# Kernel optimization log

Measured on AMD Instinct MI355X. Metric: run time of the kernel, lower is better.

The kernel has to match this reference:

```python
import jax, jax.numpy as jnp
import numpy as np

B, S, D, DA, H = 4, 2048, 1024, 1024, 16
DH = DA // H  # 64, per-head dim (tensor_split on last dim == contiguous head chunks)


def setup_inputs() -> dict:
    key = jax.random.key(0)
    ks = jax.random.split(key, 8)
    init = 0.02
    return {
        "q": jax.random.normal(ks[0], (B, S, D), jnp.float32),
        "k": jax.random.normal(ks[1], (B, S, D), jnp.float32),
        "v": jax.random.normal(ks[2], (B, S, D), jnp.float32),
        "mask": jnp.ones((B, 1, S), jnp.int32),
        "w_q": jax.random.normal(ks[3], (DA, D), jnp.float32) * init,
        "b_q": jnp.zeros((DA,), jnp.float32),
        "w_k": jax.random.normal(ks[4], (DA, D), jnp.float32) * init,
        "b_k": jnp.zeros((DA,), jnp.float32),
        "w_v": jax.random.normal(ks[5], (DA, D), jnp.float32) * init,
        "b_v": jnp.zeros((DA,), jnp.float32),
        "w_o": jax.random.normal(ks[6], (D, DA), jnp.float32) * init,
        "b_o": jnp.zeros((D,), jnp.float32),
    }


def reference(q, k, v, mask, w_q, b_q, w_k, b_k, w_v, b_v, w_o, b_o):
    # projections (nn.Linear: x @ W.T + b)
    xq = q @ w_q.T + b_q            # [B,S,DA]
    xk = k @ w_k.T + b_k
    xv = v @ w_v.T + b_v
    # tensor_split into h contiguous chunks == reshape to [B,S,H,DH]
    xq = xq.reshape(B, S, H, DH)
    xk = xk.reshape(B, S, H, DH)
    xv = xv.reshape(B, S, H, DH)
    scores = jnp.einsum('bqhd,bkhd->bhqk', xq, xk) / jnp.sqrt(jnp.asarray(DH, xq.dtype))
    # mask [B,1,S] broadcasts over heads and query rows -> [B,1,1,S]
    scores = jnp.where(mask[:, None] == 0, -jnp.inf, scores)
    probs = jax.nn.softmax(scores, axis=-1)  # dropout p=0.0 -> identity
    out = jnp.einsum('bhqk,bkhd->bqhd', probs, xv).reshape(B, S, DA)
    return out @ w_o.T + b_o        # [B,S,D]
```

## Files before the change

### kernel.cpp

```cpp
#include <hip/hip_runtime.h>
#include <hip/hip_bf16.h>
#include <cstdint>
#include <cstddef>

typedef __bf16 bf16;
typedef __attribute__((ext_vector_type(8))) __bf16 bf16x8;
typedef __attribute__((ext_vector_type(4))) __bf16 bf16x4;
typedef __attribute__((ext_vector_type(4))) float f32x4;
typedef __attribute__((ext_vector_type(4))) int i32x4;

#define MFMA_BF16(a, b, c) __builtin_amdgcn_mfma_f32_16x16x32_bf16((a), (b), (c), 0, 0, 0)

constexpr int CB = 4;
constexpr int CS = 2048;
constexpr int CD = 1024;
constexpr int CDA = 1024;
constexpr int CH = 16;
constexpr int CM = CB * CS;
constexpr int NT = CS / 64;

__global__ __launch_bounds__(256) void cvt_w4(
    const float* __restrict__ s0, const float* __restrict__ s1,
    const float* __restrict__ s2, const float* __restrict__ s3,
    bf16* __restrict__ dst)
{
    int bid = blockIdx.x;
    int m = bid >> 9;
    size_t li = ((size_t)(bid & 511) * 256 + threadIdx.x) * 8;
    const float* s = (m == 0) ? s0 : (m == 1) ? s1 : (m == 2) ? s2 : s3;
    f32x4 a = *(const f32x4*)(s + li);
    f32x4 c = *(const f32x4*)(s + li + 4);
    bf16x8 o;
#pragma unroll
    for (int j = 0; j < 4; ++j) { o[j] = (bf16)a[j]; o[4 + j] = (bf16)c[j]; }
    *(bf16x8*)(dst + (size_t)m * (CD * CDA) + li) = o;
}

struct P3 {
    const float *A0, *A1, *A2;
    const float *b0, *b1, *b2;
    bf16 *C0, *C1, *C2;
};

__global__ __launch_bounds__(512, 4) void gemm_proj(P3 p, const bf16* __restrict__ Wb)
{
    __shared__ __align__(16) char smem[49152];

    const int t = threadIdx.x;
    const int lane = t & 63;
    const int wid = t >> 6;
    const int wr = wid >> 2, wc = wid & 3;
    const int l15 = lane & 15, lg = lane >> 4;
    const int m0 = blockIdx.x * 128;
    const int n0 = blockIdx.y * 256;
    const int z = blockIdx.z;

    const float* A    = (z == 0) ? p.A0 : (z == 1) ? p.A1 : p.A2;
    const float* bias = (z == 0) ? p.b0 : (z == 1) ? p.b1 : p.b2;
    const bf16*  W    = Wb + (size_t)z * (CD * CDA);

    const int arow = t >> 2, aq = t & 3;
    const float* asrc = A + (size_t)(m0 + arow) * CD + aq * 16;
    const int aoff0 = arow * 128 + (((2 * aq) ^ (arow & 7)) << 4);
    const int aoff1 = arow * 128 + (((2 * aq + 1) ^ (arow & 7)) << 4);
    const int brow_ = wid * 8 + (lane >> 3);
    const int bcol = ((lane & 7) ^ ((lane >> 3) & 7)) << 3;

    char* Ab = smem;
    char* Bb = smem + 16384;

    f32x4 acc[4][4] = {};

    for (int ks = 0; ks < CD / 64; ++ks) {
        const int k0 = ks * 64;
        {
            f32x4 v0 = *(const f32x4*)(asrc + k0);
            f32x4 v1 = *(const f32x4*)(asrc + k0 + 4);
            bf16x8 o0;
#pragma unroll
            for (int jj = 0; jj < 4; ++jj) { o0[jj] = (bf16)v0[jj]; o0[4 + jj] = (bf16)v1[jj]; }
            *(bf16x8*)(Ab + aoff0) = o0;
        }
        {
            f32x4 v2 = *(const f32x4*)(asrc + k0 + 8);
            f32x4 v3 = *(const f32x4*)(asrc + k0 + 12);
            bf16x8 o1;
#pragma unroll
            for (int jj = 0; jj < 4; ++jj) { o1[jj] = (bf16)v2[jj]; o1[4 + jj] = (bf16)v3[jj]; }
            *(bf16x8*)(Ab + aoff1) = o1;
        }
#pragma unroll
        for (int i = 0; i < 4; ++i) {
            const bf16* src = W + (size_t)(n0 + i * 64 + brow_) * CD + k0 + bcol;
            __builtin_amdgcn_global_load_lds(
                (const __attribute__((address_space(1))) void*)src,
                (__attribute__((address_space(3))) void*)(Bb + i * 8192 + wid * 1024),
                16, 0, 0);
        }
        __syncthreads();

#pragma unroll
        for (int kk = 0; kk < 64; kk += 32) {
            bf16x8 af[4], bfv[4];
#pragma unroll
            for (int mi = 0; mi < 4; ++mi) {
                int row = wr * 64 + mi * 16 + l15;
                af[mi] = *(const bf16x8*)(Ab + row * 128 +
                                          ((((kk >> 3) + lg) ^ (row & 7)) << 4));
            }
#pragma unroll
            for (int ni = 0; ni < 4; ++ni) {
                int row = wc * 64 + ni * 16 + l15;
                bfv[ni] = *(const bf16x8*)(Bb + 128 * row +
                                           ((((kk >> 3) + lg) ^ (row & 7)) << 4));
            }
            __builtin_amdgcn_s_setprio(1);
#pragma unroll
            for (int mi = 0; mi < 4; ++mi)
#pragma unroll
                for (int ni = 0; ni < 4; ++ni)
                    acc[mi][ni] = MFMA_BF16(af[mi], bfv[ni], acc[mi][ni]);
            __builtin_amdgcn_s_setprio(0);
        }
        __syncthreads();
    }

    if (z == 2) {
        bf16* C = p.C2;
        const int mblock = m0 + wr * 64;
#pragma unroll
        for (int ni = 0; ni < 4; ++ni) {
            int n = n0 + wc * 64 + ni * 16 + l15;
            float bv = bias[n];
#pragma unroll
            for (int mi = 0; mi < 4; ++mi) {
                int s = mi * 16 + lg * 4;
                int cps = (s & 32) | ((s & 12) << 1) | ((s & 16) >> 2);
                bf16x4 o;
#pragma unroll
                for (int r = 0; r < 4; ++r) o[r] = (bf16)(acc[mi][ni][r] + bv);
                *(bf16x4*)(C + (size_t)n * CM + mblock + cps) = o;
            }
        }
    } else {
        bf16* C = (z == 0) ? p.C0 : p.C1;
#pragma unroll
        for (int ni = 0; ni < 4; ++ni) {
            int col = n0 + wc * 64 + ni * 16 + l15;
            float bv = bias[col];
#pragma unroll
            for (int mi = 0; mi < 4; ++mi)
#pragma unroll
                for (int r = 0; r < 4; ++r) {
                    int row = m0 + wr * 64 + mi * 16 + lg * 4 + r;
                    C[(size_t)row * CDA + col] = (bf16)(acc[mi][ni][r] + bv);
                }
        }
    }
}

__global__ __launch_bounds__(512, 4) void gemm_out(
    const bf16* __restrict__ A, const bf16* __restrict__ W,
    const float* __restrict__ bias, float* __restrict__ C)
{
    __shared__ __align__(16) char smem[49152];

    const int t = threadIdx.x;
    const int lane = t & 63;
    const int wid = t >> 6;
    const int wr = wid >> 2, wc = wid & 3;
    const int l15 = lane & 15, lg = lane >> 4;
    const int m0 = blockIdx.x * 128;
    const int n0 = blockIdx.y * 256;

    const int grow_ = wid * 8 + (lane >> 3);
    const int gcol = ((lane & 7) ^ ((lane >> 3) & 7)) << 3;

    char* Ab = smem;
    char* Bb = smem + 16384;

    f32x4 acc[4][4] = {};

    for (int ks = 0; ks < CDA / 64; ++ks) {
        const int k0 = ks * 64;
#pragma unroll
        for (int i = 0; i < 2; ++i) {
            const bf16* src = A + (size_t)(m0 + i * 64 + grow_) * CDA + k0 + gcol;
            __builtin_amdgcn_global_load_lds(
                (const __attribute__((address_space(1))) void*)src,
                (__attribute__((address_space(3))) void*)(Ab + i * 8192 + wid * 1024),
                16, 0, 0);
        }
#pragma unroll
        for (int i = 0; i < 4; ++i) {
            const bf16* src = W + (size_t)(n0 + i * 64 + grow_) * CDA + k0 + gcol;
            __builtin_amdgcn_global_load_lds(
                (const __attribute__((address_space(1))) void*)src,
                (__attribute__((address_space(3))) void*)(Bb + i * 8192 + wid * 1024),
                16, 0, 0);
        }
        __syncthreads();

#pragma unroll
        for (int kk = 0; kk < 64; kk += 32) {
            bf16x8 af[4], bfv[4];
#pragma unroll
            for (int mi = 0; mi < 4; ++mi) {
                int row = wr * 64 + mi * 16 + l15;
                af[mi] = *(const bf16x8*)(Ab + row * 128 +
                                          ((((kk >> 3) + lg) ^ (row & 7)) << 4));
            }
#pragma unroll
            for (int ni = 0; ni < 4; ++ni) {
                int row = wc * 64 + ni * 16 + l15;
                bfv[ni] = *(const bf16x8*)(Bb + 128 * row +
                                           ((((kk >> 3) + lg) ^ (row & 7)) << 4));
            }
            __builtin_amdgcn_s_setprio(1);
#pragma unroll
            for (int mi = 0; mi < 4; ++mi)
#pragma unroll
                for (int ni = 0; ni < 4; ++ni)
                    acc[mi][ni] = MFMA_BF16(af[mi], bfv[ni], acc[mi][ni]);
            __builtin_amdgcn_s_setprio(0);
        }
        __syncthreads();
    }

#pragma unroll
    for (int ni = 0; ni < 4; ++ni) {
        int col = n0 + wc * 64 + ni * 16 + l15;
        float bv = bias[col];
#pragma unroll
        for (int mi = 0; mi < 4; ++mi)
#pragma unroll
            for (int r = 0; r < 4; ++r) {
                int row = m0 + wr * 64 + mi * 16 + lg * 4 + r;
                C[(size_t)row * CD + col] = acc[mi][ni][r] + bv;
            }
    }
}

__global__ __launch_bounds__(512, 4) void attn_kernel(
    const bf16* __restrict__ xq, const bf16* __restrict__ xk,
    const bf16* __restrict__ xvT, const int* __restrict__ mask,
    bf16* __restrict__ out)
{
    __shared__ __align__(16) char smem[40960];
    float* Mb = (float*)(smem + 32768);

    const int t = threadIdx.x;
    const int lane = t & 63;
    const int wid = t >> 6;
    const int l15 = lane & 15, lg = lane >> 4;
    const int g = blockIdx.x;
    const int j = g >> 3;
    const int bh = (g & 7) * 8 + (j & 7);
    const int qt = j >> 3;
    const int b = bh >> 4, h = bh & 15;
    const int q0 = qt * 256;
    constexpr float SCL = 0.125f * 1.44269504088896340736f;
    constexpr float M2 = 12.0f * SCL;

    const int sub = lane >> 3;
    const int sb  = (lane & 7) ^ sub;
    const bf16* kbase = xk + (size_t)(b * CS + wid * 8 + sub) * CDA + h * 64 + sb * 8;
    const bf16* vbase = xvT + (size_t)(h * 64 + wid * 8 + sub) * CM + b * CS + sb * 8;

#define STAGE(bufi, ktt)                                                           \
    {                                                                              \
        char* Kd = smem + (bufi) * 16384 + wid * 1024;                             \
        char* Vd = smem + (bufi) * 16384 + 8192 + wid * 1024;                      \
        __builtin_amdgcn_global_load_lds(                                          \
            (const __attribute__((address_space(1))) void*)(kbase + (size_t)(ktt) * 64 * CDA), \
            (__attribute__((address_space(3))) void*)Kd, 16, 0, 0);                \
        __builtin_amdgcn_global_load_lds(                                          \
            (const __attribute__((address_space(1))) void*)(vbase + (ktt) * 64),   \
            (__attribute__((address_space(3))) void*)Vd, 16, 0, 0);                \
    }

    {
        i32x4 mk = *(const i32x4*)(mask + b * CS + t * 4);
        f32x4 o;
#pragma unroll
        for (int r = 0; r < 4; ++r) o[r] = (mk[r] == 0) ? -1.0e30f : -M2;
        *(f32x4*)(Mb + t * 4) = o;
    }

    bf16x8 aq[2][2];
#pragma unroll
    for (int mi = 0; mi < 2; ++mi)
#pragma unroll
        for (int kh = 0; kh < 2; ++kh) {
            bf16x8 v = *(const bf16x8*)(xq +
                (size_t)(b * CS + q0 + wid * 32 + mi * 16 + l15) * CDA + h * 64 + kh * 32 + lg * 8);
#pragma unroll
            for (int jj = 0; jj < 8; ++jj) v[jj] = (bf16)((float)v[jj] * SCL);
            aq[mi][kh] = v;
        }

    bf16x8 onescol;
    {
        bf16 fv = (l15 == 0) ? (bf16)1.0f : (bf16)0.0f;
#pragma unroll
        for (int jj = 0; jj < 8; ++jj) onescol[jj] = fv;
    }

    int koff[2][4], voff[2][4];
#pragma unroll
    for (int kh = 0; kh < 2; ++kh)
#pragma unroll
        for (int ni = 0; ni < 4; ++ni) {
            int key = ni * 16 + l15;
            koff[kh][ni] = key * 128 + ((kh * 64 + lg * 16) ^ ((key & 7) << 4));
        }
#pragma unroll
    for (int kks = 0; kks < 2; ++kks)
#pragma unroll
        for (int di = 0; di < 4; ++di) {
            int d = di * 16 + l15;
            voff[kks][di] = 8192 + d * 128 + ((kks * 64 + lg * 16) ^ ((d & 7) << 4));
        }

    f32x4 accO[2][5] = {};

    STAGE(0, 0);
    __syncthreads();

    for (int kt = 0; kt < NT; ++kt) {
        const int cur = kt & 1;
        char* buf = smem + cur * 16384;

        if (kt + 1 < NT) STAGE(cur ^ 1, kt + 1);

        f32x4 mb[4];
#pragma unroll
        for (int ni = 0; ni < 4; ++ni)
            mb[ni] = *(const f32x4*)(Mb + kt * 64 + ni * 16 + lg * 4);

        f32x4 sT[4][2];
#pragma unroll
        for (int ni = 0; ni < 4; ++ni) { sT[ni][0] = mb[ni]; sT[ni][1] = mb[ni]; }
#pragma unroll
        for (int kh = 0; kh < 2; ++kh) {
            bf16x8 bk[4];
#pragma unroll
            for (int ni = 0; ni < 4; ++ni)
                bk[ni] = *(const bf16x8*)(buf + koff[kh][ni]);
            __builtin_amdgcn_s_setprio(1);
#pragma unroll
            for (int ni = 0; ni < 4; ++ni)
#pragma unroll
                for (int mi = 0; mi < 2; ++mi)
                    sT[ni][mi] = MFMA_BF16(bk[ni], aq[mi][kh], sT[ni][mi]);
            __builtin_amdgcn_s_setprio(0);
        }

#pragma unroll
        for (int ni = 0; ni < 4; ++ni)
#pragma unroll
            for (int mi = 0; mi < 2; ++mi)
#pragma unroll
                for (int r = 0; r < 4; ++r)
                    sT[ni][mi][r] = exp2f(sT[ni][mi][r]);

        bf16x8 ap[2][2];
#pragma unroll
        for (int kks = 0; kks < 2; ++kks)
#pragma unroll
            for (int mi = 0; mi < 2; ++mi)
#pragma unroll
                for (int r = 0; r < 4; ++r) {
                    ap[kks][mi][r]     = (bf16)sT[2 * kks][mi][r];
                    ap[kks][mi][4 + r] = (bf16)sT[2 * kks + 1][mi][r];
                }

#pragma unroll
        for (int kks = 0; kks < 2; ++kks) {
            bf16x8 bv[4];
#pragma unroll
            for (int di = 0; di < 4; ++di)
                bv[di] = *(const bf16x8*)(buf + voff[kks][di]);
            __builtin_amdgcn_s_setprio(1);
#pragma unroll
            for (int mi = 0; mi < 2; ++mi) {
#pragma unroll
                for (int di = 0; di < 4; ++di)
                    accO[mi][di] = MFMA_BF16(ap[kks][mi], bv[di], accO[mi][di]);
                accO[mi][4] = MFMA_BF16(ap[kks][mi], onescol, accO[mi][4]);
            }
            __builtin_amdgcn_s_setprio(0);
        }

        __syncthreads();
    }
#undef STAGE

    char* Ob = smem + wid * 2048;
#pragma unroll
    for (int mi = 0; mi < 2; ++mi) {
#pragma unroll
        for (int r = 0; r < 4; ++r) {
            float lsum = __shfl(accO[mi][4][r], lane & 48);
            float inv = 1.0f / lsum;
            int qr = lg * 4 + r;
#pragma unroll
            for (int di = 0; di < 4; ++di)
                *(bf16*)(Ob + qr * 128 + (((di * 16 + l15) * 2) ^ ((qr & 7) << 4))) =
                    (bf16)(accO[mi][di][r] * inv);
        }
        __builtin_amdgcn_sched_barrier(0);
#pragma unroll
        for (int i = 0; i < 2; ++i) {
            int rr = i * 8 + (lane >> 3);
            int ch = lane & 7;
            bf16x8 o = *(const bf16x8*)(Ob + rr * 128 + ((ch * 16) ^ ((rr & 7) << 4)));
            *(bf16x8*)(out + (size_t)(b * CS + q0 + wid * 32 + mi * 16 + rr) * CDA +
                       h * 64 + ch * 8) = o;
        }
        __builtin_amdgcn_sched_barrier(0);
    }
}

extern "C" void kernel_launch(void* const* d_in, const int* in_sizes, int n_in,
                              void* d_out, int out_size, void* d_ws, size_t ws_size,
                              hipStream_t stream)
{
    const float* q   = (const float*)d_in[0];
    const float* k   = (const float*)d_in[1];
    const float* v   = (const float*)d_in[2];
    const int*   msk = (const int*)d_in[3];
    const float* w_q = (const float*)d_in[4];
    const float* b_q = (const float*)d_in[5];
    const float* w_k = (const float*)d_in[6];
    const float* b_k = (const float*)d_in[7];
    const float* w_v = (const float*)d_in[8];
    const float* b_v = (const float*)d_in[9];
    const float* w_o = (const float*)d_in[10];
    const float* b_o = (const float*)d_in[11];

    bf16* xq  = (bf16*)d_ws;
    bf16* xk  = xq + (size_t)CM * CDA;
    bf16* xvT = xk + (size_t)CM * CDA;
    bf16* at  = xvT + (size_t)CM * CDA;
    bf16* wb  = at + (size_t)CM * CDA;

    cvt_w4<<<dim3(2048), 256, 0, stream>>>(w_q, w_k, w_v, w_o, wb);

    P3 p{q, k, v, b_q, b_k, b_v, xq, xk, xvT};
    gemm_proj<<<dim3(CM / 128, CDA / 256, 3), 512, 0, stream>>>(p, wb);

    attn_kernel<<<dim3(512), 512, 0, stream>>>(xq, xk, xvT, msk, at);

    gemm_out<<<dim3(CM / 128, CD / 256), 512, 0, stream>>>(
        at, wb + 3 * (size_t)(CD * CDA), b_o, (float*)d_out);
}
```

Measured before the change: 197.4 us.

## Retile projection GEMM to 64x512 and double-buffer output GEMM LDS

The projection GEMM moves from 128x256 tiles to 64x512 tiles, with each of the 8 waves owning a 64-column strip. Each fp32 activation row is then read and converted once per 512 output columns rather than once per 256, which halves repeated A traffic and conversion work. The output GEMM gains a two-stage LDS ping-pong so the next k-slice loads while the current one is computed. The cost is larger shared memory use (72KB and 96KB) and fewer resident blocks per CU. The visible part of the output-GEMM loop does not show where the end-of-iteration synchronization sits.

```diff
diff --git a/kernel.cpp b/kernel.cpp
--- a/kernel.cpp
+++ b/kernel.cpp
@@ -44,7 +44,115 @@
 
 __global__ __launch_bounds__(512, 4) void gemm_proj(P3 p, const bf16* __restrict__ Wb)
 {
-    __shared__ __align__(16) char smem[49152];
+    __shared__ __align__(16) char smem[73728];
+
+    const int t = threadIdx.x;
+    const int lane = t & 63;
+    const int wid = t >> 6;
+    const int l15 = lane & 15, lg = lane >> 4;
+    const int m0 = blockIdx.x * 64;
+    const int n0 = blockIdx.y * 512;
+    const int z = blockIdx.z;
+
+    const float* A    = (z == 0) ? p.A0 : (z == 1) ? p.A1 : p.A2;
+    const float* bias = (z == 0) ? p.b0 : (z == 1) ? p.b1 : p.b2;
+    const bf16*  W    = Wb + (size_t)z * (CD * CDA);
+
+    const int arow = t >> 3, ac = t & 7;
+    const float* asrc = A + (size_t)(m0 + arow) * CD + ac * 8;
+    const int aoff = arow * 128 + ((ac ^ (arow & 7)) << 4);
+    const int brow_ = wid * 8 + (lane >> 3);
+    const int bcol = ((lane & 7) ^ ((lane >> 3) & 7)) << 3;
+
+    char* Ab = smem;
+    char* Bb = smem + 8192;
+
+    f32x4 acc[4][4] = {};
+
+    for (int ks = 0; ks < CD / 64; ++ks) {
+        const int k0 = ks * 64;
+        {
+            f32x4 v0 = *(const f32x4*)(asrc + k0);
+            f32x4 v1 = *(const f32x4*)(asrc + k0 + 4);
+            bf16x8 o;
+#pragma unroll
+            for (int jj = 0; jj < 4; ++jj) { o[jj] = (bf16)v0[jj]; o[4 + jj] = (bf16)v1[jj]; }
+            *(bf16x8*)(Ab + aoff) = o;
+        }
+#pragma unroll
+        for (int i = 0; i < 8; ++i) {
+            const bf16* src = W + (size_t)(n0 + i * 64 + brow_) * CD + k0 + bcol;
+            __builtin_amdgcn_global_load_lds(
+                (const __attribute__((address_space(1))) void*)src,
+                (__attribute__((address_space(3))) void*)(Bb + i * 8192 + wid * 1024),
+                16, 0, 0);
+        }
+        __syncthreads();
+
+#pragma unroll
+        for (int kk = 0; kk < 64; kk += 32) {
+            bf16x8 af[4], bfv[4];
+#pragma unroll
+            for (int mi = 0; mi < 4; ++mi) {
+                int row = mi * 16 + l15;
+                af[mi] = *(const bf16x8*)(Ab + row * 128 +
+                                          ((((kk >> 3) + lg) ^ (row & 7)) << 4));
+            }
+#pragma unroll
+            for (int ni = 0; ni < 4; ++ni) {
+                int row = wid * 64 + ni * 16 + l15;
+                bfv[ni] = *(const bf16x8*)(Bb + 128 * row +
+                                           ((((kk >> 3) + lg) ^ (row & 7)) << 4));
+            }
+            __builtin_amdgcn_s_setprio(1);
+#pragma unroll
+            for (int mi = 0; mi < 4; ++mi)
+#pragma unroll
+                for (int ni = 0; ni < 4; ++ni)
+                    acc[mi][ni] = MFMA_BF16(af[mi], bfv[ni], acc[mi][ni]);
+            __builtin_amdgcn_s_setprio(0);
+        }
+        __syncthreads();
+    }
+
+    if (z == 2) {
+        bf16* C = p.C2;
+#pragma unroll
+        for (int ni = 0; ni < 4; ++ni) {
+            int n = n0 + wid * 64 + ni * 16 + l15;
+            float bv = bias[n];
+#pragma unroll
+            for (int mi = 0; mi < 4; ++mi) {
+                int s = mi * 16 + lg * 4;
+                int cps = (s & 32) | ((s & 12) << 1) | ((s & 16) >> 2);
+                bf16x4 o;
+#pragma unroll
+                for (int r = 0; r < 4; ++r) o[r] = (bf16)(acc[mi][ni][r] + bv);
+                *(bf16x4*)(C + (size_t)n * CM + m0 + cps) = o;
+            }
+        }
+    } else {
+        bf16* C = (z == 0) ? p.C0 : p.C1;
+#pragma unroll
+        for (int ni = 0; ni < 4; ++ni) {
+            int col = n0 + wid * 64 + ni * 16 + l15;
+            float bv = bias[col];
+#pragma unroll
+            for (int mi = 0; mi < 4; ++mi)
+#pragma unroll
+                for (int r = 0; r < 4; ++r) {
+                    int row = m0 + mi * 16 + lg * 4 + r;
+                    C[(size_t)row * CDA + col] = (bf16)(acc[mi][ni][r] + bv);
+                }
+        }
+    }
+}
+
+__global__ __launch_bounds__(512, 2) void gemm_out(
+    const bf16* __restrict__ A, const bf16* __restrict__ W,
+    const float* __restrict__ bias, float* __restrict__ C)
+{
+    __shared__ __align__(16) char smem[98304];
 
     const int t = threadIdx.x;
     const int lane = t & 63;
@@ -53,136 +161,13 @@
     const int l15 = lane & 15, lg = lane >> 4;
     const int m0 = blockIdx.x * 128;
     const int n0 = blockIdx.y * 256;
-    const int z = blockIdx.z;
-
-    const float* A    = (z == 0) ? p.A0 : (z == 1) ? p.A1 : p.A2;
-    const float* bias = (z == 0) ? p.b0 : (z == 1) ? p.b1 : p.b2;
-    const bf16*  W    = Wb + (size_t)z * (CD * CDA);
-
-    const int arow = t >> 2, aq = t & 3;
-    const float* asrc = A + (size_t)(m0 + arow) * CD + aq * 16;
-    const int aoff0 = arow * 128 + (((2 * aq) ^ (arow & 7)) << 4);
-    const int aoff1 = arow * 128 + (((2 * aq + 1) ^ (arow & 7)) << 4);
-    const int brow_ = wid * 8 + (lane >> 3);
-    const int bcol = ((lane & 7) ^ ((lane >> 3) & 7)) << 3;
-
-    char* Ab = smem;
-    char* Bb = smem + 16384;
-
-    f32x4 acc[4][4] = {};
-
-    for (int ks = 0; ks < CD / 64; ++ks) {
-        const int k0 = ks * 64;
-        {
-            f32x4 v0 = *(const f32x4*)(asrc + k0);
-            f32x4 v1 = *(const f32x4*)(asrc + k0 + 4);
-            bf16x8 o0;
-#pragma unroll
-            for (int jj = 0; jj < 4; ++jj) { o0[jj] = (bf16)v0[jj]; o0[4 + jj] = (bf16)v1[jj]; }
-            *(bf16x8*)(Ab + aoff0) = o0;
-        }
-        {
-            f32x4 v2 = *(const f32x4*)(asrc + k0 + 8);
-            f32x4 v3 = *(const f32x4*)(asrc + k0 + 12);
-            bf16x8 o1;
-#pragma unroll
-            for (int jj = 0; jj < 4; ++jj) { o1[jj] = (bf16)v2[jj]; o1[4 + jj] = (bf16)v3[jj]; }
-            *(bf16x8*)(Ab + aoff1) = o1;
-        }
-#pragma unroll
-        for (int i = 0; i < 4; ++i) {
-            const bf16* src = W + (size_t)(n0 + i * 64 + brow_) * CD + k0 + bcol;
-            __builtin_amdgcn_global_load_lds(
-                (const __attribute__((address_space(1))) void*)src,
-                (__attribute__((address_space(3))) void*)(Bb + i * 8192 + wid * 1024),
-                16, 0, 0);
-        }
-        __syncthreads();
-
-#pragma unroll
-        for (int kk = 0; kk < 64; kk += 32) {
-            bf16x8 af[4], bfv[4];
-#pragma unroll
-            for (int mi = 0; mi < 4; ++mi) {
-                int row = wr * 64 + mi * 16 + l15;
-                af[mi] = *(const bf16x8*)(Ab + row * 128 +
-                                          ((((kk >> 3) + lg) ^ (row & 7)) << 4));
-            }
-#pragma unroll
-            for (int ni = 0; ni < 4; ++ni) {
-                int row = wc * 64 + ni * 16 + l15;
-                bfv[ni] = *(const bf16x8*)(Bb + 128 * row +
-                                           ((((kk >> 3) + lg) ^ (row & 7)) << 4));
-            }
-            __builtin_amdgcn_s_setprio(1);
-#pragma unroll
-            for (int mi = 0; mi < 4; ++mi)
-#pragma unroll
-                for (int ni = 0; ni < 4; ++ni)
-                    acc[mi][ni] = MFMA_BF16(af[mi], bfv[ni], acc[mi][ni]);
-            __builtin_amdgcn_s_setprio(0);
-        }
-        __syncthreads();
-    }
-
-    if (z == 2) {
-        bf16* C = p.C2;
-        const int mblock = m0 + wr * 64;
-#pragma unroll
-        for (int ni = 0; ni < 4; ++ni) {
-            int n = n0 + wc * 64 + ni * 16 + l15;
-            float bv = bias[n];
-#pragma unroll
-            for (int mi = 0; mi < 4; ++mi) {
-                int s = mi * 16 + lg * 4;
-                int cps = (s & 32) | ((s & 12) << 1) | ((s & 16) >> 2);
-                bf16x4 o;
-#pragma unroll
-                for (int r = 0; r < 4; ++r) o[r] = (bf16)(acc[mi][ni][r] + bv);
-                *(bf16x4*)(C + (size_t)n * CM + mblock + cps) = o;
-            }
-        }
-    } else {
-        bf16* C = (z == 0) ? p.C0 : p.C1;
-#pragma unroll
-        for (int ni = 0; ni < 4; ++ni) {
-            int col = n0 + wc * 64 + ni * 16 + l15;
-            float bv = bias[col];
-#pragma unroll
-            for (int mi = 0; mi < 4; ++mi)
-#pragma unroll
-                for (int r = 0; r < 4; ++r) {
-                    int row = m0 + wr * 64 + mi * 16 + lg * 4 + r;
-                    C[(size_t)row * CDA + col] = (bf16)(acc[mi][ni][r] + bv);
-                }
-        }
-    }
-}
-
-__global__ __launch_bounds__(512, 4) void gemm_out(
-    const bf16* __restrict__ A, const bf16* __restrict__ W,
-    const float* __restrict__ bias, float* __restrict__ C)
-{
-    __shared__ __align__(16) char smem[49152];
-
-    const int t = threadIdx.x;
-    const int lane = t & 63;
-    const int wid = t >> 6;
-    const int wr = wid >> 2, wc = wid & 3;
-    const int l15 = lane & 15, lg = lane >> 4;
-    const int m0 = blockIdx.x * 128;
-    const int n0 = blockIdx.y * 256;
 
     const int grow_ = wid * 8 + (lane >> 3);
     const int gcol = ((lane & 7) ^ ((lane >> 3) & 7)) << 3;
 
-    char* Ab = smem;
-    char* Bb = smem + 16384;
-
-    f32x4 acc[4][4] = {};
-
-    for (int ks = 0; ks < CDA / 64; ++ks) {
-        const int k0 = ks * 64;
+    auto STAGE = [&](int bufi, int k0) {
+        char* Ab = smem + bufi * 16384;
+        char* Bb = smem + 32768 + bufi * 32768;
 #pragma unroll
         for (int i = 0; i < 2; ++i) {
             const bf16* src = A + (size_t)(m0 + i * 64 + grow_) * CDA + k0 + gcol;
@@ -199,8 +184,18 @@
                 (__attribute__((address_space(3))) void*)(Bb + i * 8192 + wid * 1024),
                 16, 0, 0);
         }
-        __syncthreads();
-
+    };
+
+    f32x4 acc[4][4] = {};
+
+    STAGE(0, 0);
+    __syncthreads();
+
+    for (int ks = 0; ks < CDA / 64; ++ks) {
+        const int cur = ks & 1;
+        if (ks + 1 < CDA / 64) STAGE(cur ^ 1, (ks + 1) * 64);
+        char* Ab = smem + cur * 16384;
+        char* Bb = smem + 32768 + cur * 32768;
 #pragma unroll
         for (int kk = 0; kk < 64; kk += 32) {
             bf16x8 af[4], bfv[4];
@@ -448,7 +443,7 @@
     cvt_w4<<<dim3(2048), 256, 0, stream>>>(w_q, w_k, w_v, w_o, wb);
 
     P3 p{q, k, v, b_q, b_k, b_v, xq, xk, xvT};
-    gemm_proj<<<dim3(CM / 128, CDA / 256, 3), 512, 0, stream>>>(p, wb);
+    gemm_proj<<<dim3(CM / 64, CDA / 512, 3), 512, 0, stream>>>(p, wb);
 
     attn_kernel<<<dim3(512), 512, 0, stream>>>(xq, xk, xvT, msk, at);
 
```

Result: slower. 202.5 us (+2.6%).
